# Optimization experiments

Measured on AMD Instinct MI355X. Metric: run time of the kernel, lower is better.

The kernel has to match this reference:

```python
import jax, jax.numpy as jnp
import numpy as np

B, C, RXD, E, P, OSIZE = 64, 4, 64, 512, 4, 256


def setup_inputs() -> dict:
    key = jax.random.key(0)
    ks = jax.random.split(key, 6)
    x = jax.random.normal(ks[0], (B, C, RXD, E), dtype=jnp.float32)
    # rxd permutation (gather form of the one-hot permuteRxdMatrix matmul)
    rxd_perm = jax.random.permutation(ks[1], RXD)
    # E permutation and its compositions: permuter = permuter @ permuteEMatrix
    # in column-index form: idx_{p+1}[j] = idx_p[e_perm[j]]
    e_perm = np.array(jax.random.permutation(ks[2], E))
    idx = e_perm.copy()
    cols = []
    for _ in range(P):
        cols.append(idx.copy())
        idx = idx[e_perm]
    e_idx = jnp.asarray(np.stack(cols, axis=1))  # (E, P) int
    # sign selected at the single nonzero entry of each permutation column
    signs = (jax.random.uniform(ks[3], (E, P)) > 0.5).astype(jnp.float32) * 2.0 - 1.0
    fan_in = RXD * E * P
    W = jax.random.normal(ks[4], (OSIZE, fan_in), dtype=jnp.float32) / np.float32(np.sqrt(fan_in))
    b = jax.random.normal(ks[5], (OSIZE,), dtype=jnp.float32) * 0.01
    return {"x": x, "rxd_perm": rxd_perm, "e_idx": e_idx, "signs": signs, "W": W, "b": b}


def reference(x, rxd_perm, e_idx, signs, W, b):
    Bb, Cc, R, Ee = x.shape
    Pp = e_idx.shape[1]
    # permute rxd axis (exact equivalent of x.transpose @ one-hot matrix)
    out = x[:, :, rxd_perm, :]                      # (B,C,R,E)
    # signed E-permutations for all P powers (exact equiv of dense matmul
    # with permuteETensor * signTensor, which has one signed nonzero per column)
    out = out[..., e_idx] * signs                   # (B,C,R,E,P)
    L = R * Ee
    pieces = []
    for p in range(Pp):
        k = 2 ** p
        v = out[..., p].reshape(Bb, Cc, L)
        if k == 1:
            pieces.append(v)                        # pool+unpool with k=1 is identity
        else:
            Lp = ((L + k - 1) // k) * k             # ceil_mode padding
            vp = jnp.pad(v, ((0, 0), (0, 0), (0, Lp - L)), constant_values=-jnp.inf)
            w = vp.reshape(Bb, Cc, Lp // k, k)
            am = jnp.argmax(w, axis=-1)             # first max, matching torch MaxPool1d
            mx = jnp.max(w, axis=-1)
            onehot = jnp.arange(k) == am[..., None]
            # MaxUnpool: max value at argmax position, zeros elsewhere
            pieces.append(jnp.where(onehot, mx[..., None], 0.0).reshape(Bb, Cc, Lp))
    pieces[-1] = pieces[-1][:, :, :L]               # truncate last piece to L
    cat = jnp.concatenate(pieces, axis=2)           # (B,C,L*P) since L % k == 0
    return cat @ W.T + b                            # (B,C,OSIZE)
```

## Files before the change

kernel.cpp:

```cpp
#include <hip/hip_runtime.h>
#include <stdint.h>

#define B_ 64
#define C_ 4
#define R_ 64
#define E_ 512
#define P_ 4
#define OS_ 256
#define L_ (R_*E_)
#define K_ (L_*P_)
#define M_ (B_*C_)

#define BM 256
#define BN 128
#define BK 64
#define ZZ 256
#define KCH (K_/ZZ)

typedef float  floatx4 __attribute__((ext_vector_type(4)));
typedef short  shortx8 __attribute__((ext_vector_type(8)));

#define GLDS16(g, l) __builtin_amdgcn_global_load_lds(                      \
    (const __attribute__((address_space(1))) void*)(g),                     \
    (__attribute__((address_space(3))) void*)(l), 16, 0, 0)

static __device__ __forceinline__ unsigned short f2bf(float f) {
  union { float f; unsigned int u; } v; v.f = f;
  unsigned int u = v.u;
  u += 0x7fffu + ((u >> 16) & 1u);
  return (unsigned short)(u >> 16);
}

__global__ __launch_bounds__(512) void build_A(
    const float* __restrict__ x, const int* __restrict__ rxd_perm,
    const int* __restrict__ e_idx, const float* __restrict__ signs,
    unsigned short* __restrict__ A) {
  const int bcr = blockIdx.x;
  const int r  = bcr & (R_ - 1);
  const int bc = bcr >> 6;
  const int e  = threadIdx.x;
  __shared__ float xr[E_];
  xr[e] = x[((size_t)(bc * R_ + rxd_perm[r])) * E_ + e];
  __syncthreads();

  const uint4  ei = *(const uint4*)(e_idx + e * 4);
  const float4 sg = *(const float4*)(signs + e * 4);
  const float v0 = xr[ei.x] * sg.x;
  const float v1 = xr[ei.y] * sg.y;
  const float v2 = xr[ei.z] * sg.z;
  const float v3 = xr[ei.w] * sg.w;

  unsigned short* dst = A + (size_t)bc * K_ + r * E_ + e;
  dst[0] = f2bf(v0);

  {
    const float ov = __shfl_xor(v1, 1, 64);
    const bool keep = (e & 1) ? (v1 > ov) : (v1 >= ov);
    dst[L_] = f2bf(keep ? v1 : 0.0f);
  }
  {
    float m = v2; int mi = e;
    #pragma unroll
    for (int d = 1; d <= 2; d <<= 1) {
      const float om  = __shfl_xor(m, d, 64);
      const int   omi = __shfl_xor(mi, d, 64);
      const bool take = (om > m) || (om == m && omi < mi);
      m = take ? om : m; mi = take ? omi : mi;
    }
    dst[2 * L_] = f2bf((mi == e) ? v2 : 0.0f);
  }
  {
    float m = v3; int mi = e;
    #pragma unroll
    for (int d = 1; d <= 4; d <<= 1) {
      const float om  = __shfl_xor(m, d, 64);
      const int   omi = __shfl_xor(mi, d, 64);
      const bool take = (om > m) || (om == m && omi < mi);
      m = take ? om : m; mi = take ? omi : mi;
    }
    dst[3 * L_] = f2bf((mi == e) ? v3 : 0.0f);
  }
}

__global__ void init_out(const float* __restrict__ bias, float* __restrict__ out) {
  const int i = blockIdx.x * blockDim.x + threadIdx.x;
  out[i] = bias[i & (OS_ - 1)];
}

__global__ __launch_bounds__(512, 4) void gemm_splitk(
    const unsigned short* __restrict__ A, const float* __restrict__ W,
    float* __restrict__ out) {
  __shared__ unsigned short As[BM * BK];
  __shared__ unsigned short Ws[BN * BK];
  const int t    = threadIdx.x;
  const int lane = t & 63;
  const int wv   = t >> 6;

  const int id = blockIdx.x;
  const int ny = (id >> 3) & 1;
  const int z  = (id & 7) | ((id >> 4) << 3);
  const int nBase = ny * BN;
  const size_t k0base = (size_t)z * KCH;

  const int wm   = (wv >> 1) * 64;
  const int wn   = (wv & 1) * 64;
  const int lrow = lane & 15;
  const int quad = lane >> 4;
  const int rx   = lrow & 7;

  const int aCh = (lane & 7) ^ ((lane >> 3) & 7);
  floatx4 acc[4][4];
  #pragma unroll
  for (int i = 0; i < 4; ++i)
    #pragma unroll
    for (int j = 0; j < 4; ++j)
      acc[i][j] = {0.f, 0.f, 0.f, 0.f};

  for (int it = 0; it < (KCH / BK); ++it) {
    const size_t k0 = k0base + (size_t)it * BK;
    #pragma unroll
    for (int c = 0; c < 4; ++c) {
      const int sblk = (wv * 4 + c) * 64;
      const int row  = (sblk >> 3) + (lane >> 3);
      GLDS16(A + (size_t)row * K_ + k0 + aCh * 8, &As[sblk * 8]);
    }
    #pragma unroll
    for (int pass = 0; pass < 2; ++pass) {
      const int q   = pass * 512 + t;
      const int row = q >> 3, ch = q & 7;
      const float* wp = W + (size_t)(nBase + row) * K_ + k0 + ch * 8;
      const float4 a0 = *(const float4*)(wp);
      const float4 a1 = *(const float4*)(wp + 4);
      shortx8 bfv;
      bfv[0] = (short)f2bf(a0.x); bfv[1] = (short)f2bf(a0.y);
      bfv[2] = (short)f2bf(a0.z); bfv[3] = (short)f2bf(a0.w);
      bfv[4] = (short)f2bf(a1.x); bfv[5] = (short)f2bf(a1.y);
      bfv[6] = (short)f2bf(a1.z); bfv[7] = (short)f2bf(a1.w);
      *(shortx8*)(&Ws[(row * 8 + (ch ^ (row & 7))) * 8]) = bfv;
    }
    __syncthreads();

    #pragma unroll
    for (int kh = 0; kh < 2; ++kh) {
      const int ch = kh * 4 + quad;
      shortx8 af[4], wf[4];
      #pragma unroll
      for (int ti = 0; ti < 4; ++ti) {
        const int row = wm + ti * 16 + lrow;
        af[ti] = *(const shortx8*)(&As[(row * 8 + (ch ^ rx)) * 8]);
      }
      #pragma unroll
      for (int tj = 0; tj < 4; ++tj) {
        const int row = wn + tj * 16 + lrow;
        wf[tj] = *(const shortx8*)(&Ws[(row * 8 + (ch ^ rx)) * 8]);
      }
      #pragma unroll
      for (int ti = 0; ti < 4; ++ti)
        #pragma unroll
        for (int tj = 0; tj < 4; ++tj)
          acc[ti][tj] = __builtin_amdgcn_mfma_f32_16x16x32_bf16(af[ti], wf[tj], acc[ti][tj], 0, 0, 0);
    }
    __syncthreads();
  }

  #pragma unroll
  for (int ti = 0; ti < 4; ++ti)
    #pragma unroll
    for (int tj = 0; tj < 4; ++tj)
      #pragma unroll
      for (int j = 0; j < 4; ++j) {
        const int m = wm + ti * 16 + quad * 4 + j;
        const int n = nBase + wn + tj * 16 + lrow;
        atomicAdd(out + (size_t)m * OS_ + n, acc[ti][tj][j]);
      }
}

extern "C" void kernel_launch(void* const* d_in, const int* in_sizes, int n_in,
                              void* d_out, int out_size, void* d_ws, size_t ws_size,
                              hipStream_t stream) {
  const float* x        = (const float*)d_in[0];
  const int*   rxd_perm = (const int*)d_in[1];
  const int*   e_idx    = (const int*)d_in[2];
  const float* signs    = (const float*)d_in[3];
  const float* W        = (const float*)d_in[4];
  const float* bias     = (const float*)d_in[5];
  float* out = (float*)d_out;

  unsigned short* A = (unsigned short*)d_ws;

  build_A<<<dim3(B_ * C_ * R_), dim3(512), 0, stream>>>(x, rxd_perm, e_idx, signs, A);
  init_out<<<dim3((OS_ * M_) / 256), dim3(256), 0, stream>>>(bias, out);
  gemm_splitk<<<dim3(2 * ZZ), dim3(512), 0, stream>>>(A, W, out);
}
```

Measured before the change: 298.4 us.

## Double-buffer split-K GEMM, vectorize build_A, replace atomics with partial-sum reduction

build_A now handles 8 rows per block and computes the pooling argmax within each thread over 8 consecutive elements instead of with cross-lane shuffles, writing 16-byte vectors. The GEMM gets double-buffered LDS, with the next W tile loaded into registers and the next A tile staged during compute, and the split count drops from 256 to 128. Atomic adds are replaced by per-split partial buffers that a separate kernel reduces and adds bias to. This removes the atomic contention and the init kernel, at the cost of extra partial-buffer traffic, fewer blocks and higher LDS use per block.

```diff
diff --git a/kernel.cpp b/kernel.cpp
--- a/kernel.cpp
+++ b/kernel.cpp
@@ -14,8 +14,9 @@
 #define BM 256
 #define BN 128
 #define BK 64
-#define ZZ 256
-#define KCH (K_/ZZ)
+#define Z_ 128
+#define KCH (K_/Z_)
+#define ITERS (KCH/BK)
 
 typedef float  floatx4 __attribute__((ext_vector_type(4)));
 typedef short  shortx8 __attribute__((ext_vector_type(8)));
@@ -35,63 +36,82 @@
     const float* __restrict__ x, const int* __restrict__ rxd_perm,
     const int* __restrict__ e_idx, const float* __restrict__ signs,
     unsigned short* __restrict__ A) {
-  const int bcr = blockIdx.x;
-  const int r  = bcr & (R_ - 1);
-  const int bc = bcr >> 6;
-  const int e  = threadIdx.x;
-  __shared__ float xr[E_];
-  xr[e] = x[((size_t)(bc * R_ + rxd_perm[r])) * E_ + e];
+  const int blk = blockIdx.x;
+  const int bc  = blk >> 3;
+  const int rg  = blk & 7;
+  const int t   = threadIdx.x;
+  __shared__ float xr[8][E_];
+
+  #pragma unroll
+  for (int i = 0; i < 2; ++i) {
+    const int q   = i * 512 + t;
+    const int row = q >> 7;
+    const int c4  = q & 127;
+    const float4 v = *(const float4*)(
+        x + ((size_t)(bc * R_ + rxd_perm[rg * 8 + row])) * E_ + c4 * 4);
+    *(float4*)(&xr[row][c4 * 4]) = v;
+  }
   __syncthreads();
 
-  const uint4  ei = *(const uint4*)(e_idx + e * 4);
-  const float4 sg = *(const float4*)(signs + e * 4);
-  const float v0 = xr[ei.x] * sg.x;
-  const float v1 = xr[ei.y] * sg.y;
-  const float v2 = xr[ei.z] * sg.z;
-  const float v3 = xr[ei.w] * sg.w;
-
-  unsigned short* dst = A + (size_t)bc * K_ + r * E_ + e;
-  dst[0] = f2bf(v0);
+  const int rloc = t >> 6;
+  const int e0   = (t & 63) * 8;
+  const int r    = rg * 8 + rloc;
+  const float* xp = xr[rloc];
+
+  float v[4][8];
+  #pragma unroll
+  for (int i = 0; i < 8; ++i) {
+    const uint4  ei = *(const uint4*)(e_idx + (size_t)(e0 + i) * 4);
+    const float4 sg = *(const float4*)(signs + (size_t)(e0 + i) * 4);
+    v[0][i] = xp[ei.x] * sg.x;
+    v[1][i] = xp[ei.y] * sg.y;
+    v[2][i] = xp[ei.z] * sg.z;
+    v[3][i] = xp[ei.w] * sg.w;
+  }
+
+  unsigned short* dst = A + (size_t)bc * K_ + (size_t)r * E_ + e0;
+  shortx8 o;
+
+  #pragma unroll
+  for (int i = 0; i < 8; ++i) o[i] = (short)f2bf(v[0][i]);
+  *(shortx8*)(dst) = o;
+
+  #pragma unroll
+  for (int j = 0; j < 4; ++j) {
+    const float a = v[1][2 * j], b = v[1][2 * j + 1];
+    const bool first = (a >= b);
+    o[2 * j]     = (short)f2bf(first ? a : 0.0f);
+    o[2 * j + 1] = (short)f2bf(first ? 0.0f : b);
+  }
+  *(shortx8*)(dst + L_) = o;
+
+  #pragma unroll
+  for (int j = 0; j < 2; ++j) {
+    int am = 0; float m = v[2][4 * j];
+    #pragma unroll
+    for (int i = 1; i < 4; ++i)
+      if (v[2][4 * j + i] > m) { m = v[2][4 * j + i]; am = i; }
+    #pragma unroll
+    for (int i = 0; i < 4; ++i) o[4 * j + i] = (short)f2bf(i == am ? m : 0.0f);
+  }
+  *(shortx8*)(dst + 2 * L_) = o;
 
   {
-    const float ov = __shfl_xor(v1, 1, 64);
-    const bool keep = (e & 1) ? (v1 > ov) : (v1 >= ov);
-    dst[L_] = f2bf(keep ? v1 : 0.0f);
-  }
-  {
-    float m = v2; int mi = e;
-    #pragma unroll
-    for (int d = 1; d <= 2; d <<= 1) {
-      const float om  = __shfl_xor(m, d, 64);
-      const int   omi = __shfl_xor(mi, d, 64);
-      const bool take = (om > m) || (om == m && omi < mi);
-      m = take ? om : m; mi = take ? omi : mi;
-    }
-    dst[2 * L_] = f2bf((mi == e) ? v2 : 0.0f);
-  }
-  {
-    float m = v3; int mi = e;
-    #pragma unroll
-    for (int d = 1; d <= 4; d <<= 1) {
-      const float om  = __shfl_xor(m, d, 64);
-      const int   omi = __shfl_xor(mi, d, 64);
-      const bool take = (om > m) || (om == m && omi < mi);
-      m = take ? om : m; mi = take ? omi : mi;
-    }
-    dst[3 * L_] = f2bf((mi == e) ? v3 : 0.0f);
-  }
-}
-
-__global__ void init_out(const float* __restrict__ bias, float* __restrict__ out) {
-  const int i = blockIdx.x * blockDim.x + threadIdx.x;
-  out[i] = bias[i & (OS_ - 1)];
-}
-
-__global__ __launch_bounds__(512, 4) void gemm_splitk(
+    int am = 0; float m = v[3][0];
+    #pragma unroll
+    for (int i = 1; i < 8; ++i)
+      if (v[3][i] > m) { m = v[3][i]; am = i; }
+    #pragma unroll
+    for (int i = 0; i < 8; ++i) o[i] = (short)f2bf(i == am ? m : 0.0f);
+  }
+  *(shortx8*)(dst + 3 * L_) = o;
+}
+
+__global__ __launch_bounds__(512, 2) void gemm_splitk(
     const unsigned short* __restrict__ A, const float* __restrict__ W,
-    float* __restrict__ out) {
-  __shared__ unsigned short As[BM * BK];
-  __shared__ unsigned short Ws[BN * BK];
+    float* __restrict__ Pp) {
+  __shared__ unsigned short As[2][BM * BK];
+  __shared__ unsigned short Ws[2][BN * BK];
   const int t    = threadIdx.x;
   const int lane = t & 63;
   const int wv   = t >> 6;
@@ -107,39 +127,51 @@
   const int lrow = lane & 15;
   const int quad = lane >> 4;
   const int rx   = lrow & 7;
-
-  const int aCh = (lane & 7) ^ ((lane >> 3) & 7);
+  const int aCh  = (lane & 7) ^ ((lane >> 3) & 7);
+
+  const int wrow0 = t >> 3;
+  const int wch   = t & 7;
+  const float* wbase0 = W + (size_t)(nBase + wrow0) * K_ + wch * 8;
+  const float* wbase1 = wbase0 + (size_t)64 * K_;
+  const int wslot0 = (wrow0 * 8 + (wch ^ (wrow0 & 7))) * 8;
+  const int wslot1 = wslot0 + 64 * 8 * 8;
+
   floatx4 acc[4][4];
   #pragma unroll
   for (int i = 0; i < 4; ++i)
     #pragma unroll
-    for (int j = 0; j < 4; ++j)
-      acc[i][j] = {0.f, 0.f, 0.f, 0.f};
-
-  for (int it = 0; it < (KCH / BK); ++it) {
-    const size_t k0 = k0base + (size_t)it * BK;
+    for (int j = 0; j < 4; ++j) acc[i][j] = {0.f, 0.f, 0.f, 0.f};
+
+  float4 wr0, wr1, wr2, wr3;
+
+  auto loadW = [&](size_t k0) {
+    wr0 = *(const float4*)(wbase0 + k0);
+    wr1 = *(const float4*)(wbase0 + k0 + 4);
+    wr2 = *(const float4*)(wbase1 + k0);
+    wr3 = *(const float4*)(wbase1 + k0 + 4);
+  };
+  auto stageA = [&](int buf, size_t k0) {
     #pragma unroll
     for (int c = 0; c < 4; ++c) {
       const int sblk = (wv * 4 + c) * 64;
       const int row  = (sblk >> 3) + (lane >> 3);
-      GLDS16(A + (size_t)row * K_ + k0 + aCh * 8, &As[sblk * 8]);
+      GLDS16(A + (size_t)row * K_ + k0 + (size_t)aCh * 8, &As[buf][sblk * 8]);
     }
-    #pragma unroll
-    for (int pass = 0; pass < 2; ++pass) {
-      const int q   = pass * 512 + t;
-      const int row = q >> 3, ch = q & 7;
-      const float* wp = W + (size_t)(nBase + row) * K_ + k0 + ch * 8;
-      const float4 a0 = *(const float4*)(wp);
-      const float4 a1 = *(const float4*)(wp + 4);
-      shortx8 bfv;
-      bfv[0] = (short)f2bf(a0.x); bfv[1] = (short)f2bf(a0.y);
-      bfv[2] = (short)f2bf(a0.z); bfv[3] = (short)f2bf(a0.w);
-      bfv[4] = (short)f2bf(a1.x); bfv[5] = (short)f2bf(a1.y);
-      bfv[6] = (short)f2bf(a1.z); bfv[7] = (short)f2bf(a1.w);
-      *(shortx8*)(&Ws[(row * 8 + (ch ^ (row & 7))) * 8]) = bfv;
-    }
-    __syncthreads();
-
+  };
+  auto writeW = [&](int buf) {
+    shortx8 b0, b1;
+    b0[0] = (short)f2bf(wr0.x); b0[1] = (short)f2bf(wr0.y);
+    b0[2] = (short)f2bf(wr0.z); b0[3] = (short)f2bf(wr0.w);
+    b0[4] = (short)f2bf(wr1.x); b0[5] = (short)f2bf(wr1.y);
+    b0[6] = (short)f2bf(wr1.z); b0[7] = (short)f2bf(wr1.w);
+    b1[0] = (short)f2bf(wr2.x); b1[1] = (short)f2bf(wr2.y);
+    b1[2] = (short)f2bf(wr2.z); b1[3] = (short)f2bf(wr2.w);
+    b1[4] = (short)f2bf(wr3.x); b1[5] = (short)f2bf(wr3.y);
+    b1[6] = (short)f2bf(wr3.z); b1[7] = (short)f2bf(wr3.w);
+    *(shortx8*)(&Ws[buf][wslot0]) = b0;
+    *(shortx8*)(&Ws[buf][wslot1]) = b1;
+  };
+  auto compute = [&](int buf) {
     #pragma unroll
     for (int kh = 0; kh < 2; ++kh) {
       const int ch = kh * 4 + quad;
@@ -147,22 +179,42 @@
       #pragma unroll
       for (int ti = 0; ti < 4; ++ti) {
         const int row = wm + ti * 16 + lrow;
-        af[ti] = *(const shortx8*)(&As[(row * 8 + (ch ^ rx)) * 8]);
+        af[ti] = *(const shortx8*)(&As[buf][(row * 8 + (ch ^ rx)) * 8]);
       }
       #pragma unroll
       for (int tj = 0; tj < 4; ++tj) {
         const int row = wn + tj * 16 + lrow;
-        wf[tj] = *(const shortx8*)(&Ws[(row * 8 + (ch ^ rx)) * 8]);
+        wf[tj] = *(const shortx8*)(&Ws[buf][(row * 8 + (ch ^ rx)) * 8]);
       }
       #pragma unroll
       for (int ti = 0; ti < 4; ++ti)
         #pragma unroll
         for (int tj = 0; tj < 4; ++tj)
-          acc[ti][tj] = __builtin_amdgcn_mfma_f32_16x16x32_bf16(af[ti], wf[tj], acc[ti][tj], 0, 0, 0);
+          acc[ti][tj] = __builtin_amdgcn_mfma_f32_16x16x32_bf16(
+              af[ti], wf[tj], acc[ti][tj], 0, 0, 0);
     }
+  };
+
+  loadW(k0base);
+  stageA(0, k0base);
+  writeW(0);
+  __syncthreads();
+
+  #pragma unroll 2
+  for (int it = 0; it < ITERS; ++it) {
+    const int b = it & 1;
+    const bool pf = (it + 1 < ITERS);
+    if (pf) {
+      const size_t k0n = k0base + (size_t)(it + 1) * BK;
+      loadW(k0n);
+      stageA(b ^ 1, k0n);
+    }
+    compute(b);
+    if (pf) writeW(b ^ 1);
     __syncthreads();
   }
 
+  float* Pz = Pp + (size_t)z * (M_ * OS_);
   #pragma unroll
   for (int ti = 0; ti < 4; ++ti)
     #pragma unroll
@@ -171,8 +223,24 @@
       for (int j = 0; j < 4; ++j) {
         const int m = wm + ti * 16 + quad * 4 + j;
         const int n = nBase + wn + tj * 16 + lrow;
-        atomicAdd(out + (size_t)m * OS_ + n, acc[ti][tj][j]);
+        Pz[(size_t)m * OS_ + n] = acc[ti][tj][j];
       }
+}
+
+__global__ __launch_bounds__(64) void reduce_out(
+    const float* __restrict__ Pp, const float* __restrict__ bias,
+    float* __restrict__ out) {
+  const int i4 = blockIdx.x * 64 + threadIdx.x;
+  const float* p = Pp + (size_t)i4 * 4;
+  float4 s = {0.f, 0.f, 0.f, 0.f};
+  #pragma unroll 8
+  for (int zz = 0; zz < Z_; ++zz) {
+    const float4 v = *(const float4*)(p + (size_t)zz * (M_ * OS_));
+    s.x += v.x; s.y += v.y; s.z += v.z; s.w += v.w;
+  }
+  const float4 bb = *(const float4*)(bias + ((i4 * 4) & (OS_ - 1)));
+  float4 o = {s.x + bb.x, s.y + bb.y, s.z + bb.z, s.w + bb.w};
+  *(float4*)(out + (size_t)i4 * 4) = o;
 }
 
 extern "C" void kernel_launch(void* const* d_in, const int* in_sizes, int n_in,
@@ -187,8 +255,9 @@
   float* out = (float*)d_out;
 
   unsigned short* A = (unsigned short*)d_ws;
-
-  build_A<<<dim3(B_ * C_ * R_), dim3(512), 0, stream>>>(x, rxd_perm, e_idx, signs, A);
-  init_out<<<dim3((OS_ * M_) / 256), dim3(256), 0, stream>>>(bias, out);
-  gemm_splitk<<<dim3(2 * ZZ), dim3(512), 0, stream>>>(A, W, out);
-}
+  float* Pp = (float*)((char*)d_ws + (size_t)M_ * K_ * 2);
+
+  build_A<<<dim3(M_ * 8), dim3(512), 0, stream>>>(x, rxd_perm, e_idx, signs, A);
+  gemm_splitk<<<dim3(2 * Z_), dim3(512), 0, stream>>>(A, W, Pp);
+  reduce_out<<<dim3((M_ * OS_ / 4) / 64), dim3(64), 0, stream>>>(Pp, bias, out);
+}
```

Result: faster. 281.6 us (-5.6%).
